# Kernel tuning notes

Measured on AMD Instinct MI355X. Metric: run time of the kernel, lower is better.

## Reference

```python
import jax, jax.numpy as jnp
import numpy as np
import math

B, T, C, H = 4, 2048, 768, 12
HS = C // H  # 64


def setup_inputs() -> dict:
    key = jax.random.key(0)
    ks = jax.random.split(key, 6)
    s = 1.0 / math.sqrt(C)
    return {
        "x": jax.random.normal(ks[0], (B, T, C), dtype=jnp.float32),
        "memory": jax.random.normal(ks[1], (B, T, C), dtype=jnp.float32),
        "Wq": jax.random.normal(ks[2], (C, C), dtype=jnp.float32) * s,
        "bq": jnp.zeros((C,), dtype=jnp.float32),
        "Wkv": jax.random.normal(ks[3], (C, 2 * C), dtype=jnp.float32) * s,
        "bkv": jnp.zeros((2 * C,), dtype=jnp.float32),
        "Wproj": jax.random.normal(ks[4], (C, C), dtype=jnp.float32) * s,
        "bproj": jnp.zeros((C,), dtype=jnp.float32),
    }


def reference(x, memory, Wq, bq, Wkv, bkv, Wproj, bproj):
    # q projection of decoder stream x, kv projection of encoder memory
    q = x @ Wq + bq                      # [B,T,C]
    kv = memory @ Wkv + bkv              # [B,T,2C]
    k, v = jnp.split(kv, 2, axis=2)      # [B,T,C] each

    def heads(t):
        return t.reshape(B, T, H, HS).transpose(0, 2, 1, 3)  # [B,H,T,hs]

    q, k, v = heads(q), heads(k), heads(v)
    scale = 1.0 / math.sqrt(HS)
    att = jnp.einsum("bhqd,bhkd->bhqk", q, k) * scale        # [B,H,T,T]
    att = jax.nn.softmax(att, axis=-1)
    y = jnp.einsum("bhqk,bhkd->bhqd", att, v)                # [B,H,T,hs]
    y = y.transpose(0, 2, 1, 3).reshape(B, T, C)
    return y @ Wproj + bproj
```

## Files before the change

kernel.cpp:

```cpp
#include <hip/hip_runtime.h>
#include <hip/hip_bf16.h>


#define B_  4
#define T_  2048
#define C_  768
#define H_  12
#define HS_ 64

typedef __attribute__((ext_vector_type(8))) short short8;
typedef __attribute__((ext_vector_type(4))) float f32x4;

__device__ __forceinline__ short f2bf(float f) {
    __hip_bfloat16 h = __float2bfloat16(f);
    return *reinterpret_cast<short*>(&h);
}

__device__ __forceinline__ void gload_lds16(const void* g, void* l) {
    __builtin_amdgcn_global_load_lds((const __attribute__((address_space(1))) void*)g,
                                     (__attribute__((address_space(3))) void*)l,
                                     16, 0, 0);
}


__global__ void cvt2_f32_to_bf16(const float* __restrict__ a, short* __restrict__ ab,
                                 const float* __restrict__ b, short* __restrict__ bb,
                                 int n4each) {
    int i = blockIdx.x * blockDim.x + threadIdx.x;
    const float* in; short* out;
    if (i < n4each) { in = a; out = ab; }
    else            { in = b; out = bb; i -= n4each; }
    float4 v = reinterpret_cast<const float4*>(in)[i];
    short4 o;
    o.x = f2bf(v.x); o.y = f2bf(v.y); o.z = f2bf(v.z); o.w = f2bf(v.w);
    reinterpret_cast<short4*>(out)[i] = o;
}

__global__ void wtrans_tiled(const float* __restrict__ Wq,  short* __restrict__ WqT,
                             const float* __restrict__ Wkv, short* __restrict__ WkvT,
                             const float* __restrict__ Wp,  short* __restrict__ WpT,
                             float qscale) {
    __shared__ float tile[32][33];
    int bid = blockIdx.x;
    const float* in; short* out; int N; float sc = 1.0f;
    if (bid < 576)       { in = Wq;  out = WqT;  N = 768;  sc = qscale; }
    else if (bid < 1728) { in = Wkv; out = WkvT; N = 1536; bid -= 576; }
    else                 { in = Wp;  out = WpT;  N = 768;  bid -= 1728; }
    const int tiles_n = N >> 5;
    const int k0 = (bid / tiles_n) * 32;
    const int n0 = (bid % tiles_n) * 32;
    const int r = threadIdx.x >> 5;
    const int c = threadIdx.x & 31;
    #pragma unroll
    for (int i = 0; i < 4; ++i)
        tile[r + 8 * i][c] = in[(size_t)(k0 + r + 8 * i) * N + n0 + c];
    __syncthreads();
    #pragma unroll
    for (int i = 0; i < 4; ++i)
        out[(size_t)(n0 + r + 8 * i) * 768 + k0 + c] = f2bf(tile[c][r + 8 * i] * sc);
}


template<int OUT_F32, int WRITE_VT>
__device__ __forceinline__ void gemm_body(const short* __restrict__ A, const short* __restrict__ BT,
                                          const float* __restrict__ bias, void* __restrict__ out,
                                          short* __restrict__ vt,
                                          int m0, int n0, int K, int ldo, float bscale,
                                          short (*As)[64], short (*Bs)[64]) {
    const int t  = threadIdx.x;
    const int wid = t >> 6;
    const int wm = wid >> 1, wn = wid & 1;
    const int lane = t & 63;
    const int lr = lane & 15;
    const int lk = (lane >> 4) * 8;

    f32x4 acc[4][4] = {};

    const int srow = wid * 32 + (lane >> 3);
    const int scol = (lane & 7) * 8;

    for (int k0 = 0; k0 < K; k0 += 64) {
        __syncthreads();
        #pragma unroll
        for (int i = 0; i < 4; ++i)
            gload_lds16(&A[(size_t)(m0 + srow + i * 8) * K + k0 + scol],
                        &As[wid * 32 + i * 8][0]);
        #pragma unroll
        for (int i = 0; i < 4; ++i)
            gload_lds16(&BT[(size_t)(n0 + srow + i * 8) * K + k0 + scol],
                        &Bs[wid * 32 + i * 8][0]);
        __syncthreads();

        #pragma unroll
        for (int ks = 0; ks < 2; ++ks) {
            const int kk = ks * 32 + lk;
            short8 a[4], b[4];
            #pragma unroll
            for (int m = 0; m < 4; ++m)
                a[m] = *reinterpret_cast<const short8*>(&As[wm*64 + m*16 + lr][kk]);
            #pragma unroll
            for (int n = 0; n < 4; ++n)
                b[n] = *reinterpret_cast<const short8*>(&Bs[wn*64 + n*16 + lr][kk]);
            #pragma unroll
            for (int m = 0; m < 4; ++m)
                #pragma unroll
                for (int n = 0; n < 4; ++n)
                    acc[m][n] = __builtin_amdgcn_mfma_f32_16x16x32_bf16(a[m], b[n], acc[m][n], 0, 0, 0);
        }
    }

    const int rb = m0 + wm * 64;
    const int cb = n0 + wn * 64;
    const int rj = (lane >> 4) * 4;
    #pragma unroll
    for (int n = 0; n < 4; ++n) {
        const int col = cb + n * 16 + lr;
        const float bv = bias[col] * bscale;
        #pragma unroll
        for (int m = 0; m < 4; ++m) {
            #pragma unroll
            for (int j = 0; j < 4; ++j) {
                const int row = rb + m * 16 + rj + j;
                const float v = acc[m][n][j] + bv;
                if (WRITE_VT && col >= 768) {
                    const int vd = col - 768;
                    const int hh = vd >> 6, dd = vd & 63;
                    const int bb = row >> 11, tt = row & 2047;
                    const int kv = tt & 63;
                    const int slot = 32 * (kv >> 5) + 8 * ((kv >> 2) & 3)
                                   + 4 * ((kv >> 4) & 1) + (kv & 3);
                    const int ptt = (tt & ~63) | slot;
                    vt[(((size_t)bb * H_ + hh) * HS_ + dd) * T_ + ptt] = f2bf(v);
                } else if (OUT_F32) {
                    reinterpret_cast<float*>(out)[(size_t)row * ldo + col] = v;
                } else {
                    reinterpret_cast<short*>(out)[(size_t)row * ldo + col] = f2bf(v);
                }
            }
        }
    }
}

__global__ void gemm_qkv(const short* __restrict__ xb,  const short* __restrict__ memb,
                         const short* __restrict__ WqT, const short* __restrict__ WkvT,
                         const float* __restrict__ bq,  const float* __restrict__ bkv,
                         short* __restrict__ qb, short* __restrict__ kvb,
                         short* __restrict__ vt, float qscale) {
    __shared__ short As[128][64];
    __shared__ short Bs[128][64];
    const int m0 = blockIdx.y * 128;
    int bx = blockIdx.x;
    if (bx < 6) {
        gemm_body<0,0>(xb, WqT, bq, qb, nullptr, m0, bx * 128, 768, 768, qscale, As, Bs);
    } else {
        gemm_body<0,1>(memb, WkvT, bkv, kvb, vt, m0, (bx - 6) * 128, 768, 1536, 1.0f, As, Bs);
    }
}

__global__ void gemm_out(const short* __restrict__ yb, const short* __restrict__ WpT,
                         const float* __restrict__ bproj, float* __restrict__ out) {
    __shared__ short As[128][64];
    __shared__ short Bs[128][64];
    gemm_body<1,0>(yb, WpT, bproj, out, nullptr, blockIdx.y * 128, blockIdx.x * 128,
                   768, 768, 1.0f, As, Bs);
}


__global__ void __launch_bounds__(256)
attn_fwd12(const short* __restrict__ qb, const short* __restrict__ kvb,
           const short* __restrict__ vtb, short* __restrict__ yb) {
    __shared__ short Ks[64][72];
    __shared__ short Vt[64][72];

    const int id = blockIdx.x;
    const int pair = id % 48;
    const int b = pair / H_, h = pair % H_;
    const int q0 = (id / 48) * 128;
    const int t = threadIdx.x;
    const int w = t >> 6;
    const int lane = t & 63;
    const int lr = lane & 15;
    const int g = lane >> 4;

    const int str = t >> 2;
    const int stc = (t & 3) * 16;

    const short* Kb = kvb + (size_t)b * T_ * (2 * C_) + h * HS_;
    const short* Vb = vtb + (size_t)(b * H_ + h) * HS_ * T_;

    short8 aq[2][2];
    #pragma unroll
    for (int m = 0; m < 2; ++m)
        #pragma unroll
        for (int ks = 0; ks < 2; ++ks)
            aq[m][ks] = *reinterpret_cast<const short8*>(
                &qb[(size_t)(b * T_ + q0 + w * 32 + m * 16 + lr) * C_ + h * HS_ + ks * 32 + g * 8]);

    short8 ones8;
    #pragma unroll
    for (int i = 0; i < 8; ++i) ones8[i] = (short)0x3F80;

    f32x4 acc[2][4] = {};
    f32x4 accl[2] = {};

    uint4 kr0, kr1, vr0, vr1;
    {
        const short* gk = &Kb[(size_t)str * (2 * C_) + stc];
        const short* gv = &Vb[(size_t)str * T_ + stc];
        kr0 = *reinterpret_cast<const uint4*>(gk);
        kr1 = *reinterpret_cast<const uint4*>(gk + 8);
        vr0 = *reinterpret_cast<const uint4*>(gv);
        vr1 = *reinterpret_cast<const uint4*>(gv + 8);
    }

    for (int kv0 = 0; kv0 < T_; kv0 += 64) {
        __syncthreads();
        *reinterpret_cast<uint4*>(&Ks[str][stc])     = kr0;
        *reinterpret_cast<uint4*>(&Ks[str][stc + 8]) = kr1;
        *reinterpret_cast<uint4*>(&Vt[str][stc])     = vr0;
        *reinterpret_cast<uint4*>(&Vt[str][stc + 8]) = vr1;
        __syncthreads();

        if (kv0 + 64 < T_) {
            const short* gk = &Kb[(size_t)(kv0 + 64 + str) * (2 * C_) + stc];
            const short* gv = &Vb[(size_t)str * T_ + kv0 + 64 + stc];
            kr0 = *reinterpret_cast<const uint4*>(gk);
            kr1 = *reinterpret_cast<const uint4*>(gk + 8);
            vr0 = *reinterpret_cast<const uint4*>(gv);
            vr1 = *reinterpret_cast<const uint4*>(gv + 8);
        }

        f32x4 s[2][4] = {};
        #pragma unroll
        for (int ks = 0; ks < 2; ++ks) {
            #pragma unroll
            for (int n = 0; n < 4; ++n) {
                short8 bk = *reinterpret_cast<const short8*>(&Ks[n * 16 + lr][ks * 32 + g * 8]);
                #pragma unroll
                for (int m = 0; m < 2; ++m)
                    s[m][n] = __builtin_amdgcn_mfma_f32_16x16x32_bf16(bk, aq[m][ks], s[m][n], 0, 0, 0);
            }
        }

        short8 pa[2][2];
        #pragma unroll
        for (int m = 0; m < 2; ++m) {
            #pragma unroll
            for (int n = 0; n < 4; ++n) {
                #pragma unroll
                for (int j = 0; j < 4; ++j)
                    s[m][n][j] = exp2f(s[m][n][j]);
            }
            #pragma unroll
            for (int ks = 0; ks < 2; ++ks) {
                pa[m][ks][0] = f2bf(s[m][2*ks][0]); pa[m][ks][1] = f2bf(s[m][2*ks][1]);
                pa[m][ks][2] = f2bf(s[m][2*ks][2]); pa[m][ks][3] = f2bf(s[m][2*ks][3]);
                pa[m][ks][4] = f2bf(s[m][2*ks+1][0]); pa[m][ks][5] = f2bf(s[m][2*ks+1][1]);
                pa[m][ks][6] = f2bf(s[m][2*ks+1][2]); pa[m][ks][7] = f2bf(s[m][2*ks+1][3]);
            }
        }

        #pragma unroll
        for (int ks = 0; ks < 2; ++ks) {
            #pragma unroll
            for (int m = 0; m < 2; ++m)
                accl[m] = __builtin_amdgcn_mfma_f32_16x16x32_bf16(pa[m][ks], ones8, accl[m], 0, 0, 0);
            #pragma unroll
            for (int n = 0; n < 4; ++n) {
                short8 bv = *reinterpret_cast<const short8*>(&Vt[n * 16 + lr][ks * 32 + g * 8]);
                #pragma unroll
                for (int m = 0; m < 2; ++m)
                    acc[m][n] = __builtin_amdgcn_mfma_f32_16x16x32_bf16(pa[m][ks], bv, acc[m][n], 0, 0, 0);
            }
        }
    }

    #pragma unroll
    for (int m = 0; m < 2; ++m) {
        #pragma unroll
        for (int j = 0; j < 4; ++j) {
            const float inv = 1.f / accl[m][j];
            const size_t row = (size_t)(b * T_ + q0 + w * 32 + m * 16 + g * 4 + j);
            #pragma unroll
            for (int n = 0; n < 4; ++n)
                yb[row * C_ + h * HS_ + n * 16 + lr] = f2bf(acc[m][n][j] * inv);
        }
    }
}


extern "C" void kernel_launch(void* const* d_in, const int* in_sizes, int n_in,
                              void* d_out, int out_size, void* d_ws, size_t ws_size,
                              hipStream_t stream) {
    const float* x      = (const float*)d_in[0];
    const float* memory = (const float*)d_in[1];
    const float* Wq     = (const float*)d_in[2];
    const float* bq     = (const float*)d_in[3];
    const float* Wkv    = (const float*)d_in[4];
    const float* bkv    = (const float*)d_in[5];
    const float* Wproj  = (const float*)d_in[6];
    const float* bproj  = (const float*)d_in[7];

    char* ws = (char*)d_ws;
    size_t off = 0;
    auto alloc = [&](size_t bytes) { char* p = ws + off; off += (bytes + 255) & ~(size_t)255; return p; };
    short* xb   = (short*)alloc((size_t)8192 * 768 * 2);
    short* memb = (short*)alloc((size_t)8192 * 768 * 2);
    short* qb   = (short*)alloc((size_t)8192 * 768 * 2);
    short* kvb  = (short*)alloc((size_t)8192 * 1536 * 2);
    short* vtb  = (short*)alloc((size_t)B_ * H_ * HS_ * T_ * 2);
    short* WqT  = (short*)alloc((size_t)768 * 768 * 2);
    short* WkvT = (short*)alloc((size_t)1536 * 768 * 2);
    short* WpT  = (short*)alloc((size_t)768 * 768 * 2);

    const float qscale = 1.4426950408889634f / 8.0f;

    const int n4 = 8192 * 768 / 4;
    cvt2_f32_to_bf16<<<(2 * n4) / 256, 256, 0, stream>>>(x, xb, memory, memb, n4);
    wtrans_tiled<<<2304, 256, 0, stream>>>(Wq, WqT, Wkv, WkvT, Wproj, WpT, qscale);

    gemm_qkv<<<dim3(18, 64), 256, 0, stream>>>(xb, memb, WqT, WkvT, bq, bkv, qb, kvb, vtb, qscale);
    attn_fwd12<<<dim3(16 * 48), 256, 0, stream>>>(qb, kvb, vtb, xb );
    gemm_out<<<dim3(6, 64), 256, 0, stream>>>(xb, WpT, bproj, (float*)d_out);
}
```

Baseline: 181.3 us.

## Fuse prepass kernels, swizzle GEMM block order, double attention KV tile

```diff
diff --git a/kernel.cpp b/kernel.cpp
--- a/kernel.cpp
+++ b/kernel.cpp
@@ -23,25 +23,28 @@
 }
 
 
-__global__ void cvt2_f32_to_bf16(const float* __restrict__ a, short* __restrict__ ab,
-                                 const float* __restrict__ b, short* __restrict__ bb,
-                                 int n4each) {
-    int i = blockIdx.x * blockDim.x + threadIdx.x;
-    const float* in; short* out;
-    if (i < n4each) { in = a; out = ab; }
-    else            { in = b; out = bb; i -= n4each; }
-    float4 v = reinterpret_cast<const float4*>(in)[i];
-    short4 o;
-    o.x = f2bf(v.x); o.y = f2bf(v.y); o.z = f2bf(v.z); o.w = f2bf(v.w);
-    reinterpret_cast<short4*>(out)[i] = o;
-}
-
-__global__ void wtrans_tiled(const float* __restrict__ Wq,  short* __restrict__ WqT,
-                             const float* __restrict__ Wkv, short* __restrict__ WkvT,
-                             const float* __restrict__ Wp,  short* __restrict__ WpT,
-                             float qscale) {
+__global__ void prepass(const float* __restrict__ x, short* __restrict__ xb,
+                        const float* __restrict__ mem, short* __restrict__ memb,
+                        const float* __restrict__ Wq,  short* __restrict__ WqT,
+                        const float* __restrict__ Wkv, short* __restrict__ WkvT,
+                        const float* __restrict__ Wp,  short* __restrict__ WpT,
+                        float qscale) {
+    const int n4 = 8192 * 768 / 4;
+    const int cvtblocks = (2 * n4) / 256;
+    int bid = blockIdx.x;
+    if (bid < cvtblocks) {
+        int i = bid * 256 + threadIdx.x;
+        const float* in; short* out;
+        if (i < n4) { in = x; out = xb; }
+        else        { in = mem; out = memb; i -= n4; }
+        float4 v = reinterpret_cast<const float4*>(in)[i];
+        short4 o;
+        o.x = f2bf(v.x); o.y = f2bf(v.y); o.z = f2bf(v.z); o.w = f2bf(v.w);
+        reinterpret_cast<short4*>(out)[i] = o;
+        return;
+    }
     __shared__ float tile[32][33];
-    int bid = blockIdx.x;
+    bid -= cvtblocks;
     const float* in; short* out; int N; float sc = 1.0f;
     if (bid < 576)       { in = Wq;  out = WqT;  N = 768;  sc = qscale; }
     else if (bid < 1728) { in = Wkv; out = WkvT; N = 1536; bid -= 576; }
@@ -148,8 +151,10 @@
                          short* __restrict__ vt, float qscale) {
     __shared__ short As[128][64];
     __shared__ short Bs[128][64];
-    const int m0 = blockIdx.y * 128;
-    int bx = blockIdx.x;
+    const int lin = blockIdx.y * 18 + blockIdx.x;
+    const int swz = (lin % 8) * 144 + lin / 8;
+    const int bx = swz % 18;
+    const int m0 = (swz / 18) * 128;
     if (bx < 6) {
         gemm_body<0,0>(xb, WqT, bq, qb, nullptr, m0, bx * 128, 768, 768, qscale, As, Bs);
     } else {
@@ -161,16 +166,18 @@
                          const float* __restrict__ bproj, float* __restrict__ out) {
     __shared__ short As[128][64];
     __shared__ short Bs[128][64];
-    gemm_body<1,0>(yb, WpT, bproj, out, nullptr, blockIdx.y * 128, blockIdx.x * 128,
+    const int lin = blockIdx.y * 6 + blockIdx.x;
+    const int swz = (lin % 8) * 48 + lin / 8;
+    gemm_body<1,0>(yb, WpT, bproj, out, nullptr, (swz / 6) * 128, (swz % 6) * 128,
                    768, 768, 1.0f, As, Bs);
 }
 
 
 __global__ void __launch_bounds__(256)
-attn_fwd12(const short* __restrict__ qb, const short* __restrict__ kvb,
+attn_fwd13(const short* __restrict__ qb, const short* __restrict__ kvb,
            const short* __restrict__ vtb, short* __restrict__ yb) {
-    __shared__ short Ks[64][72];
-    __shared__ short Vt[64][72];
+    __shared__ short Ks[128][72];
+    __shared__ short Vt[64][136];
 
     const int id = blockIdx.x;
     const int pair = id % 48;
@@ -182,8 +189,10 @@
     const int lr = lane & 15;
     const int g = lane >> 4;
 
-    const int str = t >> 2;
-    const int stc = (t & 3) * 16;
+    const int kstr = t >> 2;
+    const int kstc = (t & 3) * 16;
+    const int vstr = t >> 2;
+    const int vstc = (t & 3) * 32;
 
     const short* Kb = kvb + (size_t)b * T_ * (2 * C_) + h * HS_;
     const short* Vb = vtb + (size_t)(b * H_ + h) * HS_ * T_;
@@ -203,74 +212,95 @@
     f32x4 acc[2][4] = {};
     f32x4 accl[2] = {};
 
-    uint4 kr0, kr1, vr0, vr1;
+    uint4 kr0, kr1, kr2, kr3, vr0, vr1, vr2, vr3;
     {
-        const short* gk = &Kb[(size_t)str * (2 * C_) + stc];
-        const short* gv = &Vb[(size_t)str * T_ + stc];
-        kr0 = *reinterpret_cast<const uint4*>(gk);
-        kr1 = *reinterpret_cast<const uint4*>(gk + 8);
+        const short* gk0 = &Kb[(size_t)kstr * (2 * C_) + kstc];
+        const short* gk1 = &Kb[(size_t)(kstr + 64) * (2 * C_) + kstc];
+        const short* gv  = &Vb[(size_t)vstr * T_ + vstc];
+        kr0 = *reinterpret_cast<const uint4*>(gk0);
+        kr1 = *reinterpret_cast<const uint4*>(gk0 + 8);
+        kr2 = *reinterpret_cast<const uint4*>(gk1);
+        kr3 = *reinterpret_cast<const uint4*>(gk1 + 8);
         vr0 = *reinterpret_cast<const uint4*>(gv);
         vr1 = *reinterpret_cast<const uint4*>(gv + 8);
-    }
-
-    for (int kv0 = 0; kv0 < T_; kv0 += 64) {
+        vr2 = *reinterpret_cast<const uint4*>(gv + 16);
+        vr3 = *reinterpret_cast<const uint4*>(gv + 24);
+    }
+
+    for (int kv0 = 0; kv0 < T_; kv0 += 128) {
         __syncthreads();
-        *reinterpret_cast<uint4*>(&Ks[str][stc])     = kr0;
-        *reinterpret_cast<uint4*>(&Ks[str][stc + 8]) = kr1;
-        *reinterpret_cast<uint4*>(&Vt[str][stc])     = vr0;
-        *reinterpret_cast<uint4*>(&Vt[str][stc + 8]) = vr1;
+        *reinterpret_cast<uint4*>(&Ks[kstr][kstc])          = kr0;
+        *reinterpret_cast<uint4*>(&Ks[kstr][kstc + 8])      = kr1;
+        *reinterpret_cast<uint4*>(&Ks[kstr + 64][kstc])     = kr2;
+        *reinterpret_cast<uint4*>(&Ks[kstr + 64][kstc + 8]) = kr3;
+        *reinterpret_cast<uint4*>(&Vt[vstr][vstc])          = vr0;
+        *reinterpret_cast<uint4*>(&Vt[vstr][vstc + 8])      = vr1;
+        *reinterpret_cast<uint4*>(&Vt[vstr][vstc + 16])     = vr2;
+        *reinterpret_cast<uint4*>(&Vt[vstr][vstc + 24])     = vr3;
         __syncthreads();
 
-        if (kv0 + 64 < T_) {
-            const short* gk = &Kb[(size_t)(kv0 + 64 + str) * (2 * C_) + stc];
-            const short* gv = &Vb[(size_t)str * T_ + kv0 + 64 + stc];
-            kr0 = *reinterpret_cast<const uint4*>(gk);
-            kr1 = *reinterpret_cast<const uint4*>(gk + 8);
+        if (kv0 + 128 < T_) {
+            const short* gk0 = &Kb[(size_t)(kv0 + 128 + kstr) * (2 * C_) + kstc];
+            const short* gk1 = &Kb[(size_t)(kv0 + 192 + kstr) * (2 * C_) + kstc];
+            const short* gv  = &Vb[(size_t)vstr * T_ + kv0 + 128 + vstc];
+            kr0 = *reinterpret_cast<const uint4*>(gk0);
+            kr1 = *reinterpret_cast<const uint4*>(gk0 + 8);
+            kr2 = *reinterpret_cast<const uint4*>(gk1);
+            kr3 = *reinterpret_cast<const uint4*>(gk1 + 8);
             vr0 = *reinterpret_cast<const uint4*>(gv);
             vr1 = *reinterpret_cast<const uint4*>(gv + 8);
-        }
-
-        f32x4 s[2][4] = {};
-        #pragma unroll
-        for (int ks = 0; ks < 2; ++ks) {
-            #pragma unroll
-            for (int n = 0; n < 4; ++n) {
-                short8 bk = *reinterpret_cast<const short8*>(&Ks[n * 16 + lr][ks * 32 + g * 8]);
+            vr2 = *reinterpret_cast<const uint4*>(gv + 16);
+            vr3 = *reinterpret_cast<const uint4*>(gv + 24);
+        }
+
+        #pragma unroll
+        for (int half = 0; half < 2; ++half) {
+            const int ho = half * 64;
+
+            f32x4 s[2][4] = {};
+            #pragma unroll
+            for (int ks = 0; ks < 2; ++ks) {
+                #pragma unroll
+                for (int n = 0; n < 4; ++n) {
+                    short8 bk = *reinterpret_cast<const short8*>(
+                        &Ks[ho + n * 16 + lr][ks * 32 + g * 8]);
+                    #pragma unroll
+                    for (int m = 0; m < 2; ++m)
+                        s[m][n] = __builtin_amdgcn_mfma_f32_16x16x32_bf16(bk, aq[m][ks], s[m][n], 0, 0, 0);
+                }
+            }
+
+            short8 pa[2][2];
+            #pragma unroll
+            for (int m = 0; m < 2; ++m) {
+                #pragma unroll
+                for (int n = 0; n < 4; ++n) {
+                    #pragma unroll
+                    for (int j = 0; j < 4; ++j)
+                        s[m][n][j] = exp2f(s[m][n][j]);
+                }
+                #pragma unroll
+                for (int ks = 0; ks < 2; ++ks) {
+                    pa[m][ks][0] = f2bf(s[m][2*ks][0]); pa[m][ks][1] = f2bf(s[m][2*ks][1]);
+                    pa[m][ks][2] = f2bf(s[m][2*ks][2]); pa[m][ks][3] = f2bf(s[m][2*ks][3]);
+                    pa[m][ks][4] = f2bf(s[m][2*ks+1][0]); pa[m][ks][5] = f2bf(s[m][2*ks+1][1]);
+                    pa[m][ks][6] = f2bf(s[m][2*ks+1][2]); pa[m][ks][7] = f2bf(s[m][2*ks+1][3]);
+                }
+            }
+
+            #pragma unroll
+            for (int ks = 0; ks < 2; ++ks) {
                 #pragma unroll
                 for (int m = 0; m < 2; ++m)
-                    s[m][n] = __builtin_amdgcn_mfma_f32_16x16x32_bf16(bk, aq[m][ks], s[m][n], 0, 0, 0);
-            }
-        }
-
-        short8 pa[2][2];
-        #pragma unroll
-        for (int m = 0; m < 2; ++m) {
-            #pragma unroll
-            for (int n = 0; n < 4; ++n) {
-                #pragma unroll
-                for (int j = 0; j < 4; ++j)
-                    s[m][n][j] = exp2f(s[m][n][j]);
-            }
-            #pragma unroll
-            for (int ks = 0; ks < 2; ++ks) {
-                pa[m][ks][0] = f2bf(s[m][2*ks][0]); pa[m][ks][1] = f2bf(s[m][2*ks][1]);
-                pa[m][ks][2] = f2bf(s[m][2*ks][2]); pa[m][ks][3] = f2bf(s[m][2*ks][3]);
-                pa[m][ks][4] = f2bf(s[m][2*ks+1][0]); pa[m][ks][5] = f2bf(s[m][2*ks+1][1]);
-                pa[m][ks][6] = f2bf(s[m][2*ks+1][2]); pa[m][ks][7] = f2bf(s[m][2*ks+1][3]);
-            }
-        }
-
-        #pragma unroll
-        for (int ks = 0; ks < 2; ++ks) {
-            #pragma unroll
-            for (int m = 0; m < 2; ++m)
-                accl[m] = __builtin_amdgcn_mfma_f32_16x16x32_bf16(pa[m][ks], ones8, accl[m], 0, 0, 0);
-            #pragma unroll
-            for (int n = 0; n < 4; ++n) {
-                short8 bv = *reinterpret_cast<const short8*>(&Vt[n * 16 + lr][ks * 32 + g * 8]);
-                #pragma unroll
-                for (int m = 0; m < 2; ++m)
-                    acc[m][n] = __builtin_amdgcn_mfma_f32_16x16x32_bf16(pa[m][ks], bv, acc[m][n], 0, 0, 0);
+                    accl[m] = __builtin_amdgcn_mfma_f32_16x16x32_bf16(pa[m][ks], ones8, accl[m], 0, 0, 0);
+                #pragma unroll
+                for (int n = 0; n < 4; ++n) {
+                    short8 bv = *reinterpret_cast<const short8*>(
+                        &Vt[n * 16 + lr][ho + ks * 32 + g * 8]);
+                    #pragma unroll
+                    for (int m = 0; m < 2; ++m)
+                        acc[m][n] = __builtin_amdgcn_mfma_f32_16x16x32_bf16(pa[m][ks], bv, acc[m][n], 0, 0, 0);
+                }
             }
         }
     }
@@ -315,11 +345,9 @@
 
     const float qscale = 1.4426950408889634f / 8.0f;
 
-    const int n4 = 8192 * 768 / 4;
-    cvt2_f32_to_bf16<<<(2 * n4) / 256, 256, 0, stream>>>(x, xb, memory, memb, n4);
-    wtrans_tiled<<<2304, 256, 0, stream>>>(Wq, WqT, Wkv, WkvT, Wproj, WpT, qscale);
-
+    prepass<<<12288 + 2304, 256, 0, stream>>>(x, xb, memory, memb,
+                                              Wq, WqT, Wkv, WkvT, Wproj, WpT, qscale);
     gemm_qkv<<<dim3(18, 64), 256, 0, stream>>>(xb, memb, WqT, WkvT, bq, bkv, qb, kvb, vtb, qscale);
-    attn_fwd12<<<dim3(16 * 48), 256, 0, stream>>>(qb, kvb, vtb, xb );
+    attn_fwd13<<<dim3(16 * 48), 256, 0, stream>>>(qb, kvb, vtb, xb );
     gemm_out<<<dim3(6, 64), 256, 0, stream>>>(xb, WpT, bproj, (float*)d_out);
 }
```

Result: no change. 178.8 us (-1.4%).
